# Kernel optimization log

Hardware: AMD Instinct MI355X
Metric: run time of the kernel (lower is better)

## Reference

```python
import jax, jax.numpy as jnp
import numpy as np

D_MODEL = 1024
NHEAD = 16
HEAD_DIM = D_MODEL // NHEAD
EPS = 1e-6


def setup_inputs() -> dict:
    key = jax.random.key(0)
    ks = jax.random.split(key, 9)
    B, S = 2, 2048
    scale = 1.0 / np.sqrt(D_MODEL)
    inp = {
        "x": jax.random.normal(ks[0], (B, S, D_MODEL), dtype=jnp.float32),
        "wq": jax.random.normal(ks[1], (D_MODEL, D_MODEL), dtype=jnp.float32) * scale,
        "bq": jnp.zeros((D_MODEL,), dtype=jnp.float32),
        "wk": jax.random.normal(ks[2], (D_MODEL, D_MODEL), dtype=jnp.float32) * scale,
        "bk": jnp.zeros((D_MODEL,), dtype=jnp.float32),
        "wv": jax.random.normal(ks[3], (D_MODEL, D_MODEL), dtype=jnp.float32) * scale,
        "bv": jnp.zeros((D_MODEL,), dtype=jnp.float32),
        "wo": jax.random.normal(ks[4], (D_MODEL, D_MODEL), dtype=jnp.float32) * scale,
        "bo": jnp.zeros((D_MODEL,), dtype=jnp.float32),
    }
    return inp


def _split_heads(x):
    B, S, _ = x.shape
    return x.reshape(B, S, NHEAD, HEAD_DIM).transpose(0, 2, 1, 3)  # [B,H,S,Dh]


def reference(x, wq, bq, wk, bk, wv, bv, wo, bo):
    # projections (torch Linear: x @ W^T + b)
    q = _split_heads(x @ wq.T + bq)
    k = _split_heads(x @ wk.T + bk)
    v = _split_heads(x @ wv.T + bv)
    # positive feature map: elu(x) + 1
    q_feat = jax.nn.elu(q) + 1.0
    k_feat = jax.nn.elu(k) + 1.0
    # dense O(n^2) kernelized scores, per original module
    scores = jnp.einsum('bhid,bhjd->bhij', q_feat, k_feat)
    denom = jnp.maximum(scores.sum(axis=-1, keepdims=True), EPS)
    weights = scores / denom  # dropout p=0 -> identity
    attended = jnp.einsum('bhij,bhjd->bhid', weights, v)
    B, H, S, Dh = attended.shape
    merged = attended.transpose(0, 2, 1, 3).reshape(B, S, H * Dh)
    return merged @ wo.T + bo
```

## Files before the change

kernel.cpp:

```cpp
#include <hip/hip_runtime.h>
#include <math.h>

#define S_LEN 2048
#define BATCH 2
#define DM 1024
#define NH 16
#define DH 64
#define EPS 1e-6f

typedef __attribute__((ext_vector_type(8))) short bf16x8;
typedef __attribute__((ext_vector_type(4))) float f32x4;

__device__ __forceinline__ unsigned short f2bf(float f) {
    unsigned u = __float_as_uint(f);
    u = (u + 0x7fffu + ((u >> 16) & 1u)) >> 16;
    return (unsigned short)u;
}
__device__ __forceinline__ float2 bf2f2(unsigned u) {
    float2 r;
    r.x = __uint_as_float(u << 16);
    r.y = __uint_as_float(u & 0xFFFF0000u);
    return r;
}
__device__ __forceinline__ void unpack8(uint4 u, float* f) {
    float2 a = bf2f2(u.x), b = bf2f2(u.y), c = bf2f2(u.z), d = bf2f2(u.w);
    f[0] = a.x; f[1] = a.y; f[2] = b.x; f[3] = b.y;
    f[4] = c.x; f[5] = c.y; f[6] = d.x; f[7] = d.y;
}
__device__ __forceinline__ void load16(const void* g, void* l) {
    __builtin_amdgcn_global_load_lds(
        (const __attribute__((address_space(1))) unsigned int*)g,
        (__attribute__((address_space(3))) unsigned int*)l,
        16, 0, 0);
}

__global__ __launch_bounds__(256) void cvt_flat(
    const float* __restrict__ x,
    const float* __restrict__ wq, const float* __restrict__ wk,
    const float* __restrict__ wv, const float* __restrict__ wo,
    unsigned short* __restrict__ x_bf,
    unsigned short* __restrict__ wq_bf, unsigned short* __restrict__ wk_bf,
    unsigned short* __restrict__ wv_bf, unsigned short* __restrict__ wo_bf)
{
    int u = blockIdx.x * 256 + threadIdx.x;
    const float* s;
    unsigned short* d;
    int off;
    if (u < 524288) {
        s = x; d = x_bf; off = u;
    } else {
        int v = u - 524288;
        int w = v >> 17;
        off = v & 131071;
        s = (w == 0) ? wq : (w == 1) ? wk : (w == 2) ? wv : wo;
        d = (w == 0) ? wq_bf : (w == 1) ? wk_bf : (w == 2) ? wv_bf : wo_bf;
    }
    float4 a = ((const float4*)s)[2 * off];
    float4 b = ((const float4*)s)[2 * off + 1];
    uint4 o;
    o.x = (unsigned)f2bf(a.x) | ((unsigned)f2bf(a.y) << 16);
    o.y = (unsigned)f2bf(a.z) | ((unsigned)f2bf(a.w) << 16);
    o.z = (unsigned)f2bf(b.x) | ((unsigned)f2bf(b.y) << 16);
    o.w = (unsigned)f2bf(b.z) | ((unsigned)f2bf(b.w) << 16);
    ((uint4*)d)[off] = o;
}

__global__ __launch_bounds__(256) void gemm_qkv(
    const unsigned short* __restrict__ A,
    const unsigned short* __restrict__ W0, const unsigned short* __restrict__ W1,
    const unsigned short* __restrict__ W2,
    const float* __restrict__ B0, const float* __restrict__ B1, const float* __restrict__ B2,
    unsigned short* __restrict__ O0, unsigned short* __restrict__ O1,
    unsigned short* __restrict__ O2,
    int M, int N, int K, int act_mask)
{
    const int z = blockIdx.z;
    const unsigned short* W = (z == 0) ? W0 : (z == 1) ? W1 : W2;
    const float* bias       = (z == 0) ? B0 : (z == 1) ? B1 : B2;
    unsigned short* O       = (z == 0) ? O0 : (z == 1) ? O1 : O2;
    const bool act = (act_mask >> z) & 1;

    __shared__ __align__(16) unsigned short AsU[128 * 64];
    __shared__ __align__(16) unsigned short BsU[128 * 64];

    const int tid = threadIdx.x;
    const int wave = tid >> 6;
    const int lane = tid & 63;
    const int quad = lane >> 4;
    const int lm = lane & 15;
    const int wr = wave >> 1, wc = wave & 1;

    const int rowBase = blockIdx.y * 128;
    const int colBase = blockIdx.x * 128;

    const int cS = (lane & 7) ^ ((lane >> 3) & 7);
    const unsigned short* Ag[4];
    const unsigned short* Wg[4];
    unsigned short* lA[4];
    unsigned short* lB[4];
#pragma unroll
    for (int i = 0; i < 4; ++i) {
        int rS = (wave * 4 + i) * 8 + (lane >> 3);
        Ag[i] = A + (size_t)(rowBase + rS) * K + cS * 8;
        Wg[i] = W + (size_t)(colBase + rS) * K + cS * 8;
        lA[i] = AsU + (size_t)((wave * 4 + i) * 64) * 8;
        lB[i] = BsU + (size_t)((wave * 4 + i) * 64) * 8;
    }

    const unsigned short* pA[4][2];
    const unsigned short* pB[4][2];
#pragma unroll
    for (int i = 0; i < 4; ++i) {
        int rA = wr * 64 + i * 16 + lm;
        int rB = wc * 64 + i * 16 + lm;
#pragma unroll
        for (int ks = 0; ks < 2; ++ks) {
            pA[i][ks] = AsU + (size_t)(rA * 8 + ((ks * 4 + quad) ^ (rA & 7))) * 8;
            pB[i][ks] = BsU + (size_t)(rB * 8 + ((ks * 4 + quad) ^ (rB & 7))) * 8;
        }
    }

    f32x4 acc[4][4];
#pragma unroll
    for (int i = 0; i < 4; ++i)
#pragma unroll
        for (int j = 0; j < 4; ++j)
            acc[i][j] = (f32x4){0.f, 0.f, 0.f, 0.f};

    for (int k0 = 0; k0 < K; k0 += 64) {
#pragma unroll
        for (int i = 0; i < 4; ++i) {
            load16(Ag[i] + k0, lA[i]);
            load16(Wg[i] + k0, lB[i]);
        }
        __syncthreads();
#pragma unroll
        for (int ks = 0; ks < 2; ++ks) {
            bf16x8 aF[4], bF[4];
#pragma unroll
            for (int i = 0; i < 4; ++i) {
                aF[i] = *(const bf16x8*)pA[i][ks];
                bF[i] = *(const bf16x8*)pB[i][ks];
            }
#pragma unroll
            for (int i = 0; i < 4; ++i)
#pragma unroll
                for (int j = 0; j < 4; ++j)
                    acc[i][j] = __builtin_amdgcn_mfma_f32_16x16x32_bf16(aF[i], bF[j], acc[i][j], 0, 0, 0);
        }
        __syncthreads();
    }

#pragma unroll
    for (int j = 0; j < 4; ++j) {
        const int col = colBase + wc * 64 + j * 16 + lm;
        const float bc = bias[col];
#pragma unroll
        for (int i = 0; i < 4; ++i) {
            const int row0 = rowBase + wr * 64 + i * 16 + quad * 4;
#pragma unroll
            for (int reg = 0; reg < 4; ++reg) {
                float v = acc[i][j][reg] + bc;
                if (act) v = (v > 0.0f) ? (v + 1.0f) : __expf(v);
                O[(size_t)(row0 + reg) * N + col] = f2bf(v);
            }
        }
    }
}

__global__ __launch_bounds__(256) void gemm_out(
    const unsigned short* __restrict__ A,
    const unsigned short* __restrict__ W,
    const float* __restrict__ bias,
    float* __restrict__ O, int M, int N, int K)
{
    __shared__ __align__(16) unsigned short AsU[64 * 64];
    __shared__ __align__(16) unsigned short BsU[128 * 64];

    const int tid = threadIdx.x;
    const int wave = tid >> 6;
    const int lane = tid & 63;
    const int quad = lane >> 4;
    const int lm = lane & 15;
    const int wr = wave >> 1, wc = wave & 1;

    const int rowBase = blockIdx.y * 64;
    const int colBase = blockIdx.x * 128;

    const int cS = (lane & 7) ^ ((lane >> 3) & 7);
    const unsigned short* Ag[2];
    const unsigned short* Wg[4];
    unsigned short* lA[2];
    unsigned short* lB[4];
#pragma unroll
    for (int i = 0; i < 2; ++i) {
        int rS = (wave * 2 + i) * 8 + (lane >> 3);
        Ag[i] = A + (size_t)(rowBase + rS) * K + cS * 8;
        lA[i] = AsU + (size_t)((wave * 2 + i) * 64) * 8;
    }
#pragma unroll
    for (int i = 0; i < 4; ++i) {
        int rS = (wave * 4 + i) * 8 + (lane >> 3);
        Wg[i] = W + (size_t)(colBase + rS) * K + cS * 8;
        lB[i] = BsU + (size_t)((wave * 4 + i) * 64) * 8;
    }

    const unsigned short* pA[2][2];
    const unsigned short* pB[4][2];
#pragma unroll
    for (int i = 0; i < 2; ++i) {
        int rA = wr * 32 + i * 16 + lm;
#pragma unroll
        for (int ks = 0; ks < 2; ++ks)
            pA[i][ks] = AsU + (size_t)(rA * 8 + ((ks * 4 + quad) ^ (rA & 7))) * 8;
    }
#pragma unroll
    for (int j = 0; j < 4; ++j) {
        int rB = wc * 64 + j * 16 + lm;
#pragma unroll
        for (int ks = 0; ks < 2; ++ks)
            pB[j][ks] = BsU + (size_t)(rB * 8 + ((ks * 4 + quad) ^ (rB & 7))) * 8;
    }

    f32x4 acc[2][4];
#pragma unroll
    for (int i = 0; i < 2; ++i)
#pragma unroll
        for (int j = 0; j < 4; ++j)
            acc[i][j] = (f32x4){0.f, 0.f, 0.f, 0.f};

    for (int k0 = 0; k0 < K; k0 += 64) {
#pragma unroll
        for (int i = 0; i < 2; ++i) load16(Ag[i] + k0, lA[i]);
#pragma unroll
        for (int i = 0; i < 4; ++i) load16(Wg[i] + k0, lB[i]);
        __syncthreads();
#pragma unroll
        for (int ks = 0; ks < 2; ++ks) {
            bf16x8 aF[2], bF[4];
#pragma unroll
            for (int i = 0; i < 2; ++i) aF[i] = *(const bf16x8*)pA[i][ks];
#pragma unroll
            for (int j = 0; j < 4; ++j) bF[j] = *(const bf16x8*)pB[j][ks];
#pragma unroll
            for (int i = 0; i < 2; ++i)
#pragma unroll
                for (int j = 0; j < 4; ++j)
                    acc[i][j] = __builtin_amdgcn_mfma_f32_16x16x32_bf16(aF[i], bF[j], acc[i][j], 0, 0, 0);
        }
        __syncthreads();
    }

#pragma unroll
    for (int j = 0; j < 4; ++j) {
        const int col = colBase + wc * 64 + j * 16 + lm;
        const float bc = bias[col];
#pragma unroll
        for (int i = 0; i < 2; ++i) {
            const int row0 = rowBase + wr * 32 + i * 16 + quad * 4;
#pragma unroll
            for (int reg = 0; reg < 4; ++reg)
                O[(size_t)(row0 + reg) * N + col] = acc[i][j][reg] + bc;
        }
    }
}

__global__ __launch_bounds__(256) void kv_part_kernel(
    const unsigned short* __restrict__ kf, const unsigned short* __restrict__ vv,
    float* __restrict__ kv_part, float* __restrict__ ksum_part)
{
    const int bh = blockIdx.x;
    const int b = bh >> 4, h = bh & 15;
    const int tid = threadIdx.x;
    const int wave = tid >> 6, lane = tid & 63;
    const int blk = blockIdx.y;
    const int posBase = (blk * 4 + wave) * 128;

    __shared__ __align__(16) float smem[17408];
    float (*Ks)[2][16][68] = (float (*)[2][16][68])smem;
    float (*Vs)[2][16][68] = (float (*)[2][16][68])(smem + 8704);

    const int pos_l = lane >> 3;
    const int f0 = (lane & 7) * 8;
    const int r0 = pos_l * 8;
    const int c0 = f0;

    float acc[8][8] = {};
    float srow[8] = {};

    for (int st = 0; st < 8; ++st) {
        const int buf = st & 1;
        size_t g0 = ((size_t)(b * S_LEN + posBase + st * 16 + pos_l)) * DM + h * DH + f0;
        size_t g1 = g0 + (size_t)8 * DM;
        uint4 ka = *(const uint4*)(kf + g0);
        uint4 kb = *(const uint4*)(kf + g1);
        uint4 va = *(const uint4*)(vv + g0);
        uint4 vb = *(const uint4*)(vv + g1);
        float kaf[8], kbf[8], vaf[8], vbf[8];
        unpack8(ka, kaf); unpack8(kb, kbf); unpack8(va, vaf); unpack8(vb, vbf);
#pragma unroll
        for (int j = 0; j < 8; ++j) srow[j] += kaf[j] + kbf[j];
        *(float4*)&Ks[wave][buf][pos_l][f0]         = make_float4(kaf[0], kaf[1], kaf[2], kaf[3]);
        *(float4*)&Ks[wave][buf][pos_l][f0 + 4]     = make_float4(kaf[4], kaf[5], kaf[6], kaf[7]);
        *(float4*)&Ks[wave][buf][pos_l + 8][f0]     = make_float4(kbf[0], kbf[1], kbf[2], kbf[3]);
        *(float4*)&Ks[wave][buf][pos_l + 8][f0 + 4] = make_float4(kbf[4], kbf[5], kbf[6], kbf[7]);
        *(float4*)&Vs[wave][buf][pos_l][f0]         = make_float4(vaf[0], vaf[1], vaf[2], vaf[3]);
        *(float4*)&Vs[wave][buf][pos_l][f0 + 4]     = make_float4(vaf[4], vaf[5], vaf[6], vaf[7]);
        *(float4*)&Vs[wave][buf][pos_l + 8][f0]     = make_float4(vbf[0], vbf[1], vbf[2], vbf[3]);
        *(float4*)&Vs[wave][buf][pos_l + 8][f0 + 4] = make_float4(vbf[4], vbf[5], vbf[6], vbf[7]);
#pragma unroll 4
        for (int q = 0; q < 16; ++q) {
            float4 a0 = *(const float4*)&Ks[wave][buf][q][r0];
            float4 a1 = *(const float4*)&Ks[wave][buf][q][r0 + 4];
            float4 b0 = *(const float4*)&Vs[wave][buf][q][c0];
            float4 b1 = *(const float4*)&Vs[wave][buf][q][c0 + 4];
            float aa[8] = {a0.x, a0.y, a0.z, a0.w, a1.x, a1.y, a1.z, a1.w};
            float bb[8] = {b0.x, b0.y, b0.z, b0.w, b1.x, b1.y, b1.z, b1.w};
#pragma unroll
            for (int i = 0; i < 8; ++i)
#pragma unroll
                for (int j = 0; j < 8; ++j)
                    acc[i][j] += aa[i] * bb[j];
        }
    }

#pragma unroll
    for (int j = 0; j < 8; ++j) {
        srow[j] += __shfl_xor(srow[j], 8);
        srow[j] += __shfl_xor(srow[j], 16);
        srow[j] += __shfl_xor(srow[j], 32);
    }

    __syncthreads();
    float* red = smem;
    float* ksred = smem + 16384;
#pragma unroll
    for (int j = 0; j < 8; ++j) {
        *(float4*)&red[wave * 4096 + (c0 + j) * 64 + r0] =
            make_float4(acc[0][j], acc[1][j], acc[2][j], acc[3][j]);
        *(float4*)&red[wave * 4096 + (c0 + j) * 64 + r0 + 4] =
            make_float4(acc[4][j], acc[5][j], acc[6][j], acc[7][j]);
    }
    if (pos_l == 0) {
        *(float4*)&ksred[wave * 64 + f0]     = make_float4(srow[0], srow[1], srow[2], srow[3]);
        *(float4*)&ksred[wave * 64 + f0 + 4] = make_float4(srow[4], srow[5], srow[6], srow[7]);
    }
    __syncthreads();

    float* outp = kv_part + ((size_t)bh * 4 + blk) * 4096;
    const int base = tid * 16;
#pragma unroll
    for (int g = 0; g < 4; ++g) {
        float4 s0 = *(const float4*)&red[base + g * 4];
        float4 s1 = *(const float4*)&red[4096 + base + g * 4];
        float4 s2 = *(const float4*)&red[8192 + base + g * 4];
        float4 s3 = *(const float4*)&red[12288 + base + g * 4];
        float4 o = make_float4(s0.x + s1.x + s2.x + s3.x,
                               s0.y + s1.y + s2.y + s3.y,
                               s0.z + s1.z + s2.z + s3.z,
                               s0.w + s1.w + s2.w + s3.w);
        *(float4*)&outp[base + g * 4] = o;
    }
    if (tid < 64) {
        float t = ksred[tid] + ksred[64 + tid] + ksred[128 + tid] + ksred[192 + tid];
        ksum_part[((size_t)bh * 4 + blk) * 64 + tid] = t;
    }
}

__global__ __launch_bounds__(256) void attend_mfma(
    const unsigned short* __restrict__ qf, const float* __restrict__ kv_part,
    const float* __restrict__ ksum_part, unsigned short* __restrict__ att)
{
    const int sBase = blockIdx.x * 128;
    const int bh = blockIdx.y;
    const int b = bh >> 4, h = bh & 15;

    __shared__ __align__(16) unsigned short Qs[128 * 64];
    __shared__ __align__(16) unsigned short Ts[64 * 64];
    __shared__ __align__(16) float ks_s[DH];
    __shared__ float den_s[128];

    const int tid = threadIdx.x;
    const int wave = tid >> 6, lane = tid & 63;
    const int quad = lane >> 4, lm = lane & 15;

#pragma unroll
    for (int i = 0; i < 4; ++i) {
        int slot = (wave * 4 + i) * 64 + lane;
        int r = slot >> 3;
        int c = (slot & 7) ^ (r & 7);
        const unsigned short* src =
            qf + ((size_t)(b * S_LEN + sBase + r)) * DM + h * DH + c * 8;
        load16(src, Qs + (size_t)(wave * 4 + i) * 512);
    }

    {
        const int e = tid >> 2, c2 = tid & 3;
        const float* kp = kv_part + (size_t)bh * 4 * 4096 + e * 64 + c2 * 16;
        float s[16];
#pragma unroll
        for (int g = 0; g < 4; ++g) {
            float4 p0 = *(const float4*)(kp + g * 4);
            float4 p1 = *(const float4*)(kp + 4096 + g * 4);
            float4 p2 = *(const float4*)(kp + 8192 + g * 4);
            float4 p3 = *(const float4*)(kp + 12288 + g * 4);
            s[g * 4 + 0] = p0.x + p1.x + p2.x + p3.x;
            s[g * 4 + 1] = p0.y + p1.y + p2.y + p3.y;
            s[g * 4 + 2] = p0.z + p1.z + p2.z + p3.z;
            s[g * 4 + 3] = p0.w + p1.w + p2.w + p3.w;
        }
        unsigned short us[16];
#pragma unroll
        for (int i = 0; i < 16; ++i) us[i] = f2bf(s[i]);
        uint4 lo, hi;
        lo.x = (unsigned)us[0]  | ((unsigned)us[1]  << 16);
        lo.y = (unsigned)us[2]  | ((unsigned)us[3]  << 16);
        lo.z = (unsigned)us[4]  | ((unsigned)us[5]  << 16);
        lo.w = (unsigned)us[6]  | ((unsigned)us[7]  << 16);
        hi.x = (unsigned)us[8]  | ((unsigned)us[9]  << 16);
        hi.y = (unsigned)us[10] | ((unsigned)us[11] << 16);
        hi.z = (unsigned)us[12] | ((unsigned)us[13] << 16);
        hi.w = (unsigned)us[14] | ((unsigned)us[15] << 16);
        const int cL = c2 * 2, cH = c2 * 2 + 1;
        *(uint4*)(Ts + (size_t)(e * 8 + (cL ^ (e & 7))) * 8) = lo;
        *(uint4*)(Ts + (size_t)(e * 8 + (cH ^ (e & 7))) * 8) = hi;
    }
    if (tid < 64) {
        const float* kq = ksum_part + (size_t)bh * 4 * 64 + tid;
        ks_s[tid] = kq[0] + kq[64] + kq[128] + kq[192];
    }
    __syncthreads();

    if (tid < 128) {
        const int r = tid;
        float d = 0.f;
#pragma unroll
        for (int cxx = 0; cxx < 8; ++cxx) {
            int slot = r * 8 + (cxx ^ (r & 7));
            uint4 u = *(const uint4*)(Qs + slot * 8);
            float f[8]; unpack8(u, f);
            const float* kss = &ks_s[cxx * 8];
#pragma unroll
            for (int j = 0; j < 8; ++j) d += f[j] * kss[j];
        }
        den_s[r] = fmaxf(d, EPS);
    }
    __syncthreads();

    f32x4 acc[2][4];
#pragma unroll
    for (int ti = 0; ti < 2; ++ti)
#pragma unroll
        for (int tj = 0; tj < 4; ++tj)
            acc[ti][tj] = (f32x4){0.f, 0.f, 0.f, 0.f};

#pragma unroll
    for (int ks_i = 0; ks_i < 2; ++ks_i) {
        bf16x8 aF[2], bF[4];
#pragma unroll
        for (int ti = 0; ti < 2; ++ti) {
            int r = wave * 32 + ti * 16 + lm;
            int cx = (ks_i * 4 + quad) ^ (r & 7);
            aF[ti] = *(const bf16x8*)(Qs + (r * 8 + cx) * 8);
        }
#pragma unroll
        for (int tj = 0; tj < 4; ++tj) {
            int e = tj * 16 + lm;
            int cx = (ks_i * 4 + quad) ^ (e & 7);
            bF[tj] = *(const bf16x8*)(Ts + (e * 8 + cx) * 8);
        }
#pragma unroll
        for (int ti = 0; ti < 2; ++ti)
#pragma unroll
            for (int tj = 0; tj < 4; ++tj)
                acc[ti][tj] = __builtin_amdgcn_mfma_f32_16x16x32_bf16(aF[ti], bF[tj], acc[ti][tj], 0, 0, 0);
    }

#pragma unroll
    for (int ti = 0; ti < 2; ++ti) {
        const int rloc0 = wave * 32 + ti * 16 + quad * 4;
#pragma unroll
        for (int reg = 0; reg < 4; ++reg) {
            float inv = 1.0f / den_s[rloc0 + reg];
            unsigned short* dst =
                att + ((size_t)(b * S_LEN + sBase + rloc0 + reg)) * DM + h * DH;
#pragma unroll
            for (int tj = 0; tj < 4; ++tj)
                dst[tj * 16 + lm] = f2bf(acc[ti][tj][reg] * inv);
        }
    }
}

extern "C" void kernel_launch(void* const* d_in, const int* in_sizes, int n_in,
                              void* d_out, int out_size, void* d_ws, size_t ws_size,
                              hipStream_t stream) {
    const float* x  = (const float*)d_in[0];
    const float* wq = (const float*)d_in[1];
    const float* bq = (const float*)d_in[2];
    const float* wk = (const float*)d_in[3];
    const float* bk = (const float*)d_in[4];
    const float* wv = (const float*)d_in[5];
    const float* bv = (const float*)d_in[6];
    const float* wo = (const float*)d_in[7];
    const float* bo = (const float*)d_in[8];
    float* out = (float*)d_out;

    const size_t ND  = (size_t)BATCH * S_LEN * DM;
    const size_t NDW = (size_t)DM * DM;
    const int BH = BATCH * NH;

    unsigned short* x_bf   = (unsigned short*)d_ws;
    unsigned short* wq_bf  = x_bf + ND;
    unsigned short* wk_bf  = wq_bf + NDW;
    unsigned short* wv_bf  = wk_bf + NDW;
    unsigned short* wo_bf  = wv_bf + NDW;
    unsigned short* qf_bf  = wo_bf + NDW;
    unsigned short* kf_bf  = qf_bf + ND;
    unsigned short* vv_bf  = kf_bf + ND;
    unsigned short* att_bf = vv_bf + ND;
    float* kv_part   = (float*)(att_bf + ND);
    float* ksum_part = kv_part + (size_t)BH * 4 * 4096;

    const int M = BATCH * S_LEN;

    cvt_flat<<<4096, 256, 0, stream>>>(x, wq, wk, wv, wo,
                                       x_bf, wq_bf, wk_bf, wv_bf, wo_bf);

    gemm_qkv<<<dim3(DM / 128, M / 128, 3), 256, 0, stream>>>(
        x_bf, wq_bf, wk_bf, wv_bf, bq, bk, bv,
        qf_bf, kf_bf, vv_bf, M, DM, DM, 0b011);

    kv_part_kernel<<<dim3(BH, 4), 256, 0, stream>>>(kf_bf, vv_bf, kv_part, ksum_part);

    attend_mfma<<<dim3(S_LEN / 128, BH), 256, 0, stream>>>(qf_bf, kv_part, ksum_part, att_bf);

    gemm_out<<<dim3(DM / 128, M / 64), 256, 0, stream>>>(
        att_bf, wo_bf, bo, out, M, DM, DM);
}
```

Baseline: 171.9 us.

## Fuse linear-attention apply into output projection GEMM with per-head recompute

Replaces the separate attend kernel and output GEMM with one kernel. For each head it computes the normalized Q·KV tile into shared memory and immediately multiplies it by the matching Wo slice, accumulating the final output. A small reduce kernel precomputes the bf16 KV matrices and key sums. This avoids writing and re-reading the attended activation buffer, at the cost of recomputing the per-head attend for every output column block and adding extra barriers per head iteration.

```diff
diff --git a/kernel.cpp b/kernel.cpp
--- a/kernel.cpp
+++ b/kernel.cpp
@@ -168,103 +168,6 @@
     }
 }
 
-__global__ __launch_bounds__(256) void gemm_out(
-    const unsigned short* __restrict__ A,
-    const unsigned short* __restrict__ W,
-    const float* __restrict__ bias,
-    float* __restrict__ O, int M, int N, int K)
-{
-    __shared__ __align__(16) unsigned short AsU[64 * 64];
-    __shared__ __align__(16) unsigned short BsU[128 * 64];
-
-    const int tid = threadIdx.x;
-    const int wave = tid >> 6;
-    const int lane = tid & 63;
-    const int quad = lane >> 4;
-    const int lm = lane & 15;
-    const int wr = wave >> 1, wc = wave & 1;
-
-    const int rowBase = blockIdx.y * 64;
-    const int colBase = blockIdx.x * 128;
-
-    const int cS = (lane & 7) ^ ((lane >> 3) & 7);
-    const unsigned short* Ag[2];
-    const unsigned short* Wg[4];
-    unsigned short* lA[2];
-    unsigned short* lB[4];
-#pragma unroll
-    for (int i = 0; i < 2; ++i) {
-        int rS = (wave * 2 + i) * 8 + (lane >> 3);
-        Ag[i] = A + (size_t)(rowBase + rS) * K + cS * 8;
-        lA[i] = AsU + (size_t)((wave * 2 + i) * 64) * 8;
-    }
-#pragma unroll
-    for (int i = 0; i < 4; ++i) {
-        int rS = (wave * 4 + i) * 8 + (lane >> 3);
-        Wg[i] = W + (size_t)(colBase + rS) * K + cS * 8;
-        lB[i] = BsU + (size_t)((wave * 4 + i) * 64) * 8;
-    }
-
-    const unsigned short* pA[2][2];
-    const unsigned short* pB[4][2];
-#pragma unroll
-    for (int i = 0; i < 2; ++i) {
-        int rA = wr * 32 + i * 16 + lm;
-#pragma unroll
-        for (int ks = 0; ks < 2; ++ks)
-            pA[i][ks] = AsU + (size_t)(rA * 8 + ((ks * 4 + quad) ^ (rA & 7))) * 8;
-    }
-#pragma unroll
-    for (int j = 0; j < 4; ++j) {
-        int rB = wc * 64 + j * 16 + lm;
-#pragma unroll
-        for (int ks = 0; ks < 2; ++ks)
-            pB[j][ks] = BsU + (size_t)(rB * 8 + ((ks * 4 + quad) ^ (rB & 7))) * 8;
-    }
-
-    f32x4 acc[2][4];
-#pragma unroll
-    for (int i = 0; i < 2; ++i)
-#pragma unroll
-        for (int j = 0; j < 4; ++j)
-            acc[i][j] = (f32x4){0.f, 0.f, 0.f, 0.f};
-
-    for (int k0 = 0; k0 < K; k0 += 64) {
-#pragma unroll
-        for (int i = 0; i < 2; ++i) load16(Ag[i] + k0, lA[i]);
-#pragma unroll
-        for (int i = 0; i < 4; ++i) load16(Wg[i] + k0, lB[i]);
-        __syncthreads();
-#pragma unroll
-        for (int ks = 0; ks < 2; ++ks) {
-            bf16x8 aF[2], bF[4];
-#pragma unroll
-            for (int i = 0; i < 2; ++i) aF[i] = *(const bf16x8*)pA[i][ks];
-#pragma unroll
-            for (int j = 0; j < 4; ++j) bF[j] = *(const bf16x8*)pB[j][ks];
-#pragma unroll
-            for (int i = 0; i < 2; ++i)
-#pragma unroll
-                for (int j = 0; j < 4; ++j)
-                    acc[i][j] = __builtin_amdgcn_mfma_f32_16x16x32_bf16(aF[i], bF[j], acc[i][j], 0, 0, 0);
-        }
-        __syncthreads();
-    }
-
-#pragma unroll
-    for (int j = 0; j < 4; ++j) {
-        const int col = colBase + wc * 64 + j * 16 + lm;
-        const float bc = bias[col];
-#pragma unroll
-        for (int i = 0; i < 2; ++i) {
-            const int row0 = rowBase + wr * 32 + i * 16 + quad * 4;
-#pragma unroll
-            for (int reg = 0; reg < 4; ++reg)
-                O[(size_t)(row0 + reg) * N + col] = acc[i][j][reg] + bc;
-        }
-    }
-}
-
 __global__ __launch_bounds__(256) void kv_part_kernel(
     const unsigned short* __restrict__ kf, const unsigned short* __restrict__ vv,
     float* __restrict__ kv_part, float* __restrict__ ksum_part)
@@ -367,126 +270,226 @@
     }
 }
 
-__global__ __launch_bounds__(256) void attend_mfma(
-    const unsigned short* __restrict__ qf, const float* __restrict__ kv_part,
-    const float* __restrict__ ksum_part, unsigned short* __restrict__ att)
+__global__ __launch_bounds__(256) void kv_reduce_kernel(
+    const float* __restrict__ kv_part, const float* __restrict__ ksum_part,
+    unsigned short* __restrict__ kvT_bf, float* __restrict__ ksum)
 {
-    const int sBase = blockIdx.x * 128;
-    const int bh = blockIdx.y;
-    const int b = bh >> 4, h = bh & 15;
-
-    __shared__ __align__(16) unsigned short Qs[128 * 64];
+    const int bh = blockIdx.x;
+    const int tid = threadIdx.x;
+    const float* base = kv_part + (size_t)bh * 4 * 4096 + tid * 16;
+    float s[16];
+#pragma unroll
+    for (int g = 0; g < 4; ++g) {
+        float4 p0 = *(const float4*)(base + g * 4);
+        float4 p1 = *(const float4*)(base + 4096 + g * 4);
+        float4 p2 = *(const float4*)(base + 8192 + g * 4);
+        float4 p3 = *(const float4*)(base + 12288 + g * 4);
+        s[g * 4 + 0] = p0.x + p1.x + p2.x + p3.x;
+        s[g * 4 + 1] = p0.y + p1.y + p2.y + p3.y;
+        s[g * 4 + 2] = p0.z + p1.z + p2.z + p3.z;
+        s[g * 4 + 3] = p0.w + p1.w + p2.w + p3.w;
+    }
+    unsigned short us[16];
+#pragma unroll
+    for (int i = 0; i < 16; ++i) us[i] = f2bf(s[i]);
+    uint4 o0, o1;
+    o0.x = (unsigned)us[0]  | ((unsigned)us[1]  << 16);
+    o0.y = (unsigned)us[2]  | ((unsigned)us[3]  << 16);
+    o0.z = (unsigned)us[4]  | ((unsigned)us[5]  << 16);
+    o0.w = (unsigned)us[6]  | ((unsigned)us[7]  << 16);
+    o1.x = (unsigned)us[8]  | ((unsigned)us[9]  << 16);
+    o1.y = (unsigned)us[10] | ((unsigned)us[11] << 16);
+    o1.z = (unsigned)us[12] | ((unsigned)us[13] << 16);
+    o1.w = (unsigned)us[14] | ((unsigned)us[15] << 16);
+    uint4* dst = (uint4*)(kvT_bf + (size_t)bh * (DH * DH) + tid * 16);
+    dst[0] = o0; dst[1] = o1;
+    if (tid < DH) {
+        const float* kq = ksum_part + (size_t)bh * 4 * 64 + tid;
+        ksum[bh * DH + tid] = kq[0] + kq[64] + kq[128] + kq[192];
+    }
+}
+
+__global__ __launch_bounds__(256) void attend_out(
+    const unsigned short* __restrict__ qf,
+    const unsigned short* __restrict__ kvT,
+    const float* __restrict__ ksum,
+    const unsigned short* __restrict__ wo,
+    const float* __restrict__ bo,
+    float* __restrict__ out)
+{
+    const int rowBase = blockIdx.y * 64;
+    const int colBase = blockIdx.x * 128;
+    const int b = blockIdx.y >> 5;
+
+    __shared__ __align__(16) unsigned short Qs[64 * 64];
     __shared__ __align__(16) unsigned short Ts[64 * 64];
-    __shared__ __align__(16) float ks_s[DH];
-    __shared__ float den_s[128];
+    __shared__ __align__(16) unsigned short Ws[128 * 64];
+    __shared__ __align__(16) unsigned short Ps[64 * 64];
+    __shared__ __align__(16) float ks_s[64];
+    __shared__ float den_part[4][64];
 
     const int tid = threadIdx.x;
     const int wave = tid >> 6, lane = tid & 63;
     const int quad = lane >> 4, lm = lane & 15;
-
+    const int wr = wave >> 1, wc = wave & 1;
+
+    const unsigned short* qSrc[2];
+    unsigned short* qDst[2];
+    const unsigned short* tSrc[2];
+    unsigned short* tDst[2];
+    const unsigned short* wSrc[4];
+    unsigned short* wDst[4];
+#pragma unroll
+    for (int i = 0; i < 2; ++i) {
+        int slot = (wave * 2 + i) * 64 + lane;
+        int r = slot >> 3, c = (slot & 7) ^ (r & 7);
+        qSrc[i] = qf + (size_t)(rowBase + r) * DM + c * 8;
+        qDst[i] = Qs + (size_t)((wave * 2 + i) * 64) * 8;
+        tSrc[i] = kvT + (size_t)(b * NH) * (DH * DH) + r * DH + c * 8;
+        tDst[i] = Ts + (size_t)((wave * 2 + i) * 64) * 8;
+    }
 #pragma unroll
     for (int i = 0; i < 4; ++i) {
         int slot = (wave * 4 + i) * 64 + lane;
-        int r = slot >> 3;
-        int c = (slot & 7) ^ (r & 7);
-        const unsigned short* src =
-            qf + ((size_t)(b * S_LEN + sBase + r)) * DM + h * DH + c * 8;
-        load16(src, Qs + (size_t)(wave * 4 + i) * 512);
-    }
-
+        int r = slot >> 3, c = (slot & 7) ^ (r & 7);
+        wSrc[i] = wo + (size_t)(colBase + r) * DM + c * 8;
+        wDst[i] = Ws + (size_t)((wave * 4 + i) * 64) * 8;
+    }
+
+    const unsigned short* pQ[2];
+    const unsigned short* pT[4][2];
     {
-        const int e = tid >> 2, c2 = tid & 3;
-        const float* kp = kv_part + (size_t)bh * 4 * 4096 + e * 64 + c2 * 16;
-        float s[16];
-#pragma unroll
-        for (int g = 0; g < 4; ++g) {
-            float4 p0 = *(const float4*)(kp + g * 4);
-            float4 p1 = *(const float4*)(kp + 4096 + g * 4);
-            float4 p2 = *(const float4*)(kp + 8192 + g * 4);
-            float4 p3 = *(const float4*)(kp + 12288 + g * 4);
-            s[g * 4 + 0] = p0.x + p1.x + p2.x + p3.x;
-            s[g * 4 + 1] = p0.y + p1.y + p2.y + p3.y;
-            s[g * 4 + 2] = p0.z + p1.z + p2.z + p3.z;
-            s[g * 4 + 3] = p0.w + p1.w + p2.w + p3.w;
-        }
-        unsigned short us[16];
-#pragma unroll
-        for (int i = 0; i < 16; ++i) us[i] = f2bf(s[i]);
-        uint4 lo, hi;
-        lo.x = (unsigned)us[0]  | ((unsigned)us[1]  << 16);
-        lo.y = (unsigned)us[2]  | ((unsigned)us[3]  << 16);
-        lo.z = (unsigned)us[4]  | ((unsigned)us[5]  << 16);
-        lo.w = (unsigned)us[6]  | ((unsigned)us[7]  << 16);
-        hi.x = (unsigned)us[8]  | ((unsigned)us[9]  << 16);
-        hi.y = (unsigned)us[10] | ((unsigned)us[11] << 16);
-        hi.z = (unsigned)us[12] | ((unsigned)us[13] << 16);
-        hi.w = (unsigned)us[14] | ((unsigned)us[15] << 16);
-        const int cL = c2 * 2, cH = c2 * 2 + 1;
-        *(uint4*)(Ts + (size_t)(e * 8 + (cL ^ (e & 7))) * 8) = lo;
-        *(uint4*)(Ts + (size_t)(e * 8 + (cH ^ (e & 7))) * 8) = hi;
-    }
-    if (tid < 64) {
-        const float* kq = ksum_part + (size_t)bh * 4 * 64 + tid;
-        ks_s[tid] = kq[0] + kq[64] + kq[128] + kq[192];
-    }
-    __syncthreads();
-
-    if (tid < 128) {
-        const int r = tid;
-        float d = 0.f;
-#pragma unroll
-        for (int cxx = 0; cxx < 8; ++cxx) {
-            int slot = r * 8 + (cxx ^ (r & 7));
-            uint4 u = *(const uint4*)(Qs + slot * 8);
-            float f[8]; unpack8(u, f);
-            const float* kss = &ks_s[cxx * 8];
-#pragma unroll
-            for (int j = 0; j < 8; ++j) d += f[j] * kss[j];
-        }
-        den_s[r] = fmaxf(d, EPS);
-    }
-    __syncthreads();
-
-    f32x4 acc[2][4];
-#pragma unroll
-    for (int ti = 0; ti < 2; ++ti)
-#pragma unroll
-        for (int tj = 0; tj < 4; ++tj)
-            acc[ti][tj] = (f32x4){0.f, 0.f, 0.f, 0.f};
-
-#pragma unroll
-    for (int ks_i = 0; ks_i < 2; ++ks_i) {
-        bf16x8 aF[2], bF[4];
-#pragma unroll
-        for (int ti = 0; ti < 2; ++ti) {
-            int r = wave * 32 + ti * 16 + lm;
-            int cx = (ks_i * 4 + quad) ^ (r & 7);
-            aF[ti] = *(const bf16x8*)(Qs + (r * 8 + cx) * 8);
-        }
+        int r = wave * 16 + lm;
+#pragma unroll
+        for (int ks = 0; ks < 2; ++ks)
+            pQ[ks] = Qs + (size_t)(r * 8 + ((ks * 4 + quad) ^ (r & 7))) * 8;
 #pragma unroll
         for (int tj = 0; tj < 4; ++tj) {
             int e = tj * 16 + lm;
-            int cx = (ks_i * 4 + quad) ^ (e & 7);
-            bF[tj] = *(const bf16x8*)(Ts + (e * 8 + cx) * 8);
-        }
-#pragma unroll
-        for (int ti = 0; ti < 2; ++ti)
-#pragma unroll
-            for (int tj = 0; tj < 4; ++tj)
-                acc[ti][tj] = __builtin_amdgcn_mfma_f32_16x16x32_bf16(aF[ti], bF[tj], acc[ti][tj], 0, 0, 0);
-    }
-
-#pragma unroll
-    for (int ti = 0; ti < 2; ++ti) {
-        const int rloc0 = wave * 32 + ti * 16 + quad * 4;
+#pragma unroll
+            for (int ks = 0; ks < 2; ++ks)
+                pT[tj][ks] = Ts + (size_t)(e * 8 + ((ks * 4 + quad) ^ (e & 7))) * 8;
+        }
+    }
+    const unsigned short* pP[2][2];
+    const unsigned short* pW[4][2];
+#pragma unroll
+    for (int i = 0; i < 2; ++i) {
+        int r = wr * 32 + i * 16 + lm;
+#pragma unroll
+        for (int ks = 0; ks < 2; ++ks)
+            pP[i][ks] = Ps + (size_t)(r * 8 + ((ks * 4 + quad) ^ (r & 7))) * 8;
+    }
+#pragma unroll
+    for (int j = 0; j < 4; ++j) {
+        int n = wc * 64 + j * 16 + lm;
+#pragma unroll
+        for (int ks = 0; ks < 2; ++ks)
+            pW[j][ks] = Ws + (size_t)(n * 8 + ((ks * 4 + quad) ^ (n & 7))) * 8;
+    }
+
+    const int ds = tid & 63, dq = tid >> 6;
+    const unsigned short* dQ0 = Qs + (size_t)(ds * 8 + ((dq * 2) ^ (ds & 7))) * 8;
+    const unsigned short* dQ1 = Qs + (size_t)(ds * 8 + ((dq * 2 + 1) ^ (ds & 7))) * 8;
+
+    unsigned short* sP[4][4];
+#pragma unroll
+    for (int reg = 0; reg < 4; ++reg) {
+        int srow = wave * 16 + quad * 4 + reg;
+#pragma unroll
+        for (int tj = 0; tj < 4; ++tj) {
+            int e = tj * 16 + lm;
+            sP[reg][tj] = Ps + (size_t)(srow * 8 + ((e >> 3) ^ (srow & 7))) * 8 + (e & 7);
+        }
+    }
+
+    f32x4 oacc[2][4];
+#pragma unroll
+    for (int i = 0; i < 2; ++i)
+#pragma unroll
+        for (int j = 0; j < 4; ++j)
+            oacc[i][j] = (f32x4){0.f, 0.f, 0.f, 0.f};
+
+    for (int h = 0; h < NH; ++h) {
+#pragma unroll
+        for (int i = 0; i < 2; ++i) {
+            load16(qSrc[i] + h * DH, qDst[i]);
+            load16(tSrc[i] + h * (DH * DH), tDst[i]);
+        }
+#pragma unroll
+        for (int i = 0; i < 4; ++i)
+            load16(wSrc[i] + h * DH, wDst[i]);
+        if (tid < 16)
+            *(float4*)&ks_s[tid * 4] =
+                *(const float4*)&ksum[(b * NH + h) * DH + tid * 4];
+        __syncthreads();
+
+        {
+            uint4 u0 = *(const uint4*)dQ0;
+            uint4 u1 = *(const uint4*)dQ1;
+            float f0[8], f1[8];
+            unpack8(u0, f0); unpack8(u1, f1);
+            const float* kss = &ks_s[dq * 16];
+            float d = 0.f;
+#pragma unroll
+            for (int j = 0; j < 8; ++j) d += f0[j] * kss[j] + f1[j] * kss[8 + j];
+            den_part[dq][ds] = d;
+        }
+
+        f32x4 pacc[4];
+#pragma unroll
+        for (int tj = 0; tj < 4; ++tj) pacc[tj] = (f32x4){0.f, 0.f, 0.f, 0.f};
+#pragma unroll
+        for (int ks = 0; ks < 2; ++ks) {
+            bf16x8 aF = *(const bf16x8*)pQ[ks];
+#pragma unroll
+            for (int tj = 0; tj < 4; ++tj) {
+                bf16x8 bF = *(const bf16x8*)pT[tj][ks];
+                pacc[tj] = __builtin_amdgcn_mfma_f32_16x16x32_bf16(aF, bF, pacc[tj], 0, 0, 0);
+            }
+        }
+        __syncthreads();
+
+        float inv[4];
 #pragma unroll
         for (int reg = 0; reg < 4; ++reg) {
-            float inv = 1.0f / den_s[rloc0 + reg];
-            unsigned short* dst =
-                att + ((size_t)(b * S_LEN + sBase + rloc0 + reg)) * DM + h * DH;
-#pragma unroll
-            for (int tj = 0; tj < 4; ++tj)
-                dst[tj * 16 + lm] = f2bf(acc[ti][tj][reg] * inv);
+            int srow = wave * 16 + quad * 4 + reg;
+            float den = den_part[0][srow] + den_part[1][srow] +
+                        den_part[2][srow] + den_part[3][srow];
+            inv[reg] = 1.0f / fmaxf(den, EPS);
+        }
+#pragma unroll
+        for (int tj = 0; tj < 4; ++tj)
+#pragma unroll
+            for (int reg = 0; reg < 4; ++reg)
+                *sP[reg][tj] = f2bf(pacc[tj][reg] * inv[reg]);
+        __syncthreads();
+
+#pragma unroll
+        for (int ks = 0; ks < 2; ++ks) {
+            bf16x8 aF[2], bF[4];
+#pragma unroll
+            for (int i = 0; i < 2; ++i) aF[i] = *(const bf16x8*)pP[i][ks];
+#pragma unroll
+            for (int j = 0; j < 4; ++j) bF[j] = *(const bf16x8*)pW[j][ks];
+#pragma unroll
+            for (int i = 0; i < 2; ++i)
+#pragma unroll
+                for (int j = 0; j < 4; ++j)
+                    oacc[i][j] = __builtin_amdgcn_mfma_f32_16x16x32_bf16(aF[i], bF[j], oacc[i][j], 0, 0, 0);
+        }
+    }
+
+#pragma unroll
+    for (int j = 0; j < 4; ++j) {
+        const int col = colBase + wc * 64 + j * 16 + lm;
+        const float bc = bo[col];
+#pragma unroll
+        for (int i = 0; i < 2; ++i) {
+            const int row0 = rowBase + wr * 32 + i * 16 + quad * 4;
+#pragma unroll
+            for (int reg = 0; reg < 4; ++reg)
+                out[(size_t)(row0 + reg) * DM + col] = oacc[i][j][reg] + bc;
         }
     }
 }
@@ -517,9 +520,10 @@
     unsigned short* qf_bf  = wo_bf + NDW;
     unsigned short* kf_bf  = qf_bf + ND;
     unsigned short* vv_bf  = kf_bf + ND;
-    unsigned short* att_bf = vv_bf + ND;
-    float* kv_part   = (float*)(att_bf + ND);
+    unsigned short* kvT_bf = vv_bf + ND;
+    float* kv_part   = (float*)(kvT_bf + (size_t)BH * DH * DH);
     float* ksum_part = kv_part + (size_t)BH * 4 * 4096;
+    float* ksum      = ksum_part + (size_t)BH * 4 * 64;
 
     const int M = BATCH * S_LEN;
 
@@ -532,8 +536,8 @@
 
     kv_part_kernel<<<dim3(BH, 4), 256, 0, stream>>>(kf_bf, vv_bf, kv_part, ksum_part);
 
-    attend_mfma<<<dim3(S_LEN / 128, BH), 256, 0, stream>>>(qf_bf, kv_part, ksum_part, att_bf);
-
-    gemm_out<<<dim3(DM / 128, M / 64), 256, 0, stream>>>(
-        att_bf, wo_bf, bo, out, M, DM, DM);
-}
+    kv_reduce_kernel<<<BH, 256, 0, stream>>>(kv_part, ksum_part, kvT_bf, ksum);
+
+    attend_out<<<dim3(DM / 128, M / 64), 256, 0, stream>>>(
+        qf_bf, kvT_bf, ksum, wo_bf, bo, out);
+}
```

Result: slower. 178.8 us (+4.0%).

## Fuse Q/K/V projections into one GEMM sharing the activation tile

Applied to the files above, without the earlier changes.

Replaces the z-indexed QKV GEMM (three separate 128x128 tile grids) with a single kernel where each block loads one 128-row activation tile and computes 64-column outputs for all three weight matrices. This reuses the A tile across Q, K and V, cutting activation reloads from global memory and LDS. In exchange the block count stays at 512 rather than 768, accumulator registers per thread grow from 16 to 24 f32x4, and each wave now owns 32 rows by 64 columns per projection, which may lower occupancy.

```diff
diff --git a/kernel.cpp b/kernel.cpp
--- a/kernel.cpp
+++ b/kernel.cpp
@@ -65,104 +65,123 @@
     ((uint4*)d)[off] = o;
 }
 
-__global__ __launch_bounds__(256) void gemm_qkv(
+__global__ __launch_bounds__(256) void gemm_qkv3(
     const unsigned short* __restrict__ A,
     const unsigned short* __restrict__ W0, const unsigned short* __restrict__ W1,
     const unsigned short* __restrict__ W2,
     const float* __restrict__ B0, const float* __restrict__ B1, const float* __restrict__ B2,
     unsigned short* __restrict__ O0, unsigned short* __restrict__ O1,
-    unsigned short* __restrict__ O2,
-    int M, int N, int K, int act_mask)
+    unsigned short* __restrict__ O2)
 {
-    const int z = blockIdx.z;
-    const unsigned short* W = (z == 0) ? W0 : (z == 1) ? W1 : W2;
-    const float* bias       = (z == 0) ? B0 : (z == 1) ? B1 : B2;
-    unsigned short* O       = (z == 0) ? O0 : (z == 1) ? O1 : O2;
-    const bool act = (act_mask >> z) & 1;
-
     __shared__ __align__(16) unsigned short AsU[128 * 64];
-    __shared__ __align__(16) unsigned short BsU[128 * 64];
+    __shared__ __align__(16) unsigned short WsU[3][64 * 64];
 
     const int tid = threadIdx.x;
     const int wave = tid >> 6;
     const int lane = tid & 63;
     const int quad = lane >> 4;
     const int lm = lane & 15;
-    const int wr = wave >> 1, wc = wave & 1;
 
     const int rowBase = blockIdx.y * 128;
-    const int colBase = blockIdx.x * 128;
+    const int colBase = blockIdx.x * 64;
 
     const int cS = (lane & 7) ^ ((lane >> 3) & 7);
     const unsigned short* Ag[4];
-    const unsigned short* Wg[4];
     unsigned short* lA[4];
-    unsigned short* lB[4];
 #pragma unroll
     for (int i = 0; i < 4; ++i) {
         int rS = (wave * 4 + i) * 8 + (lane >> 3);
-        Ag[i] = A + (size_t)(rowBase + rS) * K + cS * 8;
-        Wg[i] = W + (size_t)(colBase + rS) * K + cS * 8;
+        Ag[i] = A + (size_t)(rowBase + rS) * DM + cS * 8;
         lA[i] = AsU + (size_t)((wave * 4 + i) * 64) * 8;
-        lB[i] = BsU + (size_t)((wave * 4 + i) * 64) * 8;
-    }
-
-    const unsigned short* pA[4][2];
-    const unsigned short* pB[4][2];
-#pragma unroll
-    for (int i = 0; i < 4; ++i) {
-        int rA = wr * 64 + i * 16 + lm;
-        int rB = wc * 64 + i * 16 + lm;
+    }
+    const unsigned short* Wg[3][2];
+    unsigned short* lB[3][2];
+#pragma unroll
+    for (int i = 0; i < 2; ++i) {
+        int rS = (wave * 2 + i) * 8 + (lane >> 3);
+        Wg[0][i] = W0 + (size_t)(colBase + rS) * DM + cS * 8;
+        Wg[1][i] = W1 + (size_t)(colBase + rS) * DM + cS * 8;
+        Wg[2][i] = W2 + (size_t)(colBase + rS) * DM + cS * 8;
+#pragma unroll
+        for (int z = 0; z < 3; ++z)
+            lB[z][i] = WsU[z] + (size_t)((wave * 2 + i) * 64) * 8;
+    }
+
+    const unsigned short* pA[2][2];
+#pragma unroll
+    for (int i = 0; i < 2; ++i) {
+        int rA = wave * 32 + i * 16 + lm;
+#pragma unroll
+        for (int ks = 0; ks < 2; ++ks)
+            pA[i][ks] = AsU + (size_t)(rA * 8 + ((ks * 4 + quad) ^ (rA & 7))) * 8;
+    }
+    const unsigned short* pB[3][4][2];
+#pragma unroll
+    for (int z = 0; z < 3; ++z)
+#pragma unroll
+        for (int j = 0; j < 4; ++j) {
+            int n = j * 16 + lm;
+#pragma unroll
+            for (int ks = 0; ks < 2; ++ks)
+                pB[z][j][ks] = WsU[z] + (size_t)(n * 8 + ((ks * 4 + quad) ^ (n & 7))) * 8;
+        }
+
+    f32x4 acc[3][2][4];
+#pragma unroll
+    for (int z = 0; z < 3; ++z)
+#pragma unroll
+        for (int i = 0; i < 2; ++i)
+#pragma unroll
+            for (int j = 0; j < 4; ++j)
+                acc[z][i][j] = (f32x4){0.f, 0.f, 0.f, 0.f};
+
+    for (int k0 = 0; k0 < DM; k0 += 64) {
+#pragma unroll
+        for (int i = 0; i < 4; ++i) load16(Ag[i] + k0, lA[i]);
+#pragma unroll
+        for (int z = 0; z < 3; ++z)
+#pragma unroll
+            for (int i = 0; i < 2; ++i) load16(Wg[z][i] + k0, lB[z][i]);
+        __syncthreads();
 #pragma unroll
         for (int ks = 0; ks < 2; ++ks) {
-            pA[i][ks] = AsU + (size_t)(rA * 8 + ((ks * 4 + quad) ^ (rA & 7))) * 8;
-            pB[i][ks] = BsU + (size_t)(rB * 8 + ((ks * 4 + quad) ^ (rB & 7))) * 8;
-        }
-    }
-
-    f32x4 acc[4][4];
-#pragma unroll
-    for (int i = 0; i < 4; ++i)
-#pragma unroll
-        for (int j = 0; j < 4; ++j)
-            acc[i][j] = (f32x4){0.f, 0.f, 0.f, 0.f};
-
-    for (int k0 = 0; k0 < K; k0 += 64) {
-#pragma unroll
-        for (int i = 0; i < 4; ++i) {
-            load16(Ag[i] + k0, lA[i]);
-            load16(Wg[i] + k0, lB[i]);
+            bf16x8 aF[2];
+#pragma unroll
+            for (int i = 0; i < 2; ++i) aF[i] = *(const bf16x8*)pA[i][ks];
+#pragma unroll
+            for (int z = 0; z < 3; ++z) {
+                bf16x8 bF[4];
+#pragma unroll
+                for (int j = 0; j < 4; ++j) bF[j] = *(const bf16x8*)pB[z][j][ks];
+#pragma unroll
+                for (int i = 0; i < 2; ++i)
+#pragma unroll
+                    for (int j = 0; j < 4; ++j)
+                        acc[z][i][j] = __builtin_amdgcn_mfma_f32_16x16x32_bf16(
+                            aF[i], bF[j], acc[z][i][j], 0, 0, 0);
+            }
         }
         __syncthreads();
-#pragma unroll
-        for (int ks = 0; ks < 2; ++ks) {
-            bf16x8 aF[4], bF[4];
-#pragma unroll
-            for (int i = 0; i < 4; ++i) {
-                aF[i] = *(const bf16x8*)pA[i][ks];
-                bF[i] = *(const bf16x8*)pB[i][ks];
-            }
-#pragma unroll
-            for (int i = 0; i < 4; ++i)
-#pragma unroll
-                for (int j = 0; j < 4; ++j)
-                    acc[i][j] = __builtin_amdgcn_mfma_f32_16x16x32_bf16(aF[i], bF[j], acc[i][j], 0, 0, 0);
-        }
-        __syncthreads();
-    }
-
-#pragma unroll
-    for (int j = 0; j < 4; ++j) {
-        const int col = colBase + wc * 64 + j * 16 + lm;
-        const float bc = bias[col];
-#pragma unroll
-        for (int i = 0; i < 4; ++i) {
-            const int row0 = rowBase + wr * 64 + i * 16 + quad * 4;
-#pragma unroll
-            for (int reg = 0; reg < 4; ++reg) {
-                float v = acc[i][j][reg] + bc;
-                if (act) v = (v > 0.0f) ? (v + 1.0f) : __expf(v);
-                O[(size_t)(row0 + reg) * N + col] = f2bf(v);
+    }
+
+#pragma unroll
+    for (int z = 0; z < 3; ++z) {
+        const float* bias = (z == 0) ? B0 : (z == 1) ? B1 : B2;
+        unsigned short* O = (z == 0) ? O0 : (z == 1) ? O1 : O2;
+        const bool act = (z < 2);
+#pragma unroll
+        for (int j = 0; j < 4; ++j) {
+            const int col = colBase + j * 16 + lm;
+            const float bc = bias[col];
+#pragma unroll
+            for (int i = 0; i < 2; ++i) {
+                const int row0 = rowBase + wave * 32 + i * 16 + quad * 4;
+#pragma unroll
+                for (int reg = 0; reg < 4; ++reg) {
+                    float v = acc[z][i][j][reg] + bc;
+                    if (act) v = (v > 0.0f) ? (v + 1.0f) : __expf(v);
+                    O[(size_t)(row0 + reg) * DM + col] = f2bf(v);
+                }
             }
         }
     }
@@ -526,9 +545,8 @@
     cvt_flat<<<4096, 256, 0, stream>>>(x, wq, wk, wv, wo,
                                        x_bf, wq_bf, wk_bf, wv_bf, wo_bf);
 
-    gemm_qkv<<<dim3(DM / 128, M / 128, 3), 256, 0, stream>>>(
-        x_bf, wq_bf, wk_bf, wv_bf, bq, bk, bv,
-        qf_bf, kf_bf, vv_bf, M, DM, DM, 0b011);
+    gemm_qkv3<<<dim3(DM / 64, M / 128), 256, 0, stream>>>(
+        x_bf, wq_bf, wk_bf, wv_bf, bq, bk, bv, qf_bf, kf_bf, vv_bf);
 
     kv_part_kernel<<<dim3(BH, 4), 256, 0, stream>>>(kf_bf, vv_bf, kv_part, ksum_part);
 
```

Result: slower. 193.3 us (+12.4%).
